# Kernel tuning notes

Measured on AMD Instinct MI355X. Metric: run time of the kernel, lower is better.

Reference implementation:

```python
import jax, jax.numpy as jnp
import numpy as np

N_STUDENT = 100000
N_COURSE = 20000
N_EDGES = 1000000
HIDDEN = 128


def setup_inputs() -> dict:
    key = jax.random.key(0)
    ks = jax.random.split(key, 8)
    scale = 1.0 / np.sqrt(2 * HIDDEN)
    return {
        "z_student": jax.random.normal(ks[0], (N_STUDENT, HIDDEN), dtype=jnp.float32),
        "z_course": jax.random.normal(ks[1], (N_COURSE, HIDDEN), dtype=jnp.float32),
        "row": jax.random.randint(ks[2], (N_EDGES,), 0, N_STUDENT, dtype=jnp.int64),
        "col": jax.random.randint(ks[3], (N_EDGES,), 0, N_COURSE, dtype=jnp.int64),
        "W1": jax.random.normal(ks[4], (2 * HIDDEN, HIDDEN), dtype=jnp.float32) * scale,
        "b1": jnp.zeros((HIDDEN,), dtype=jnp.float32),
        "W2": jax.random.normal(ks[5], (HIDDEN, 1), dtype=jnp.float32) * (1.0 / np.sqrt(HIDDEN)),
        "b2": jnp.zeros((1,), dtype=jnp.float32),
    }


def reference(z_student, z_course, row, col, W1, b1, W2, b2):
    # gather endpoint embeddings and concat along feature dim: [E, 2H]
    z = jnp.concatenate([z_student[row], z_course[col]], axis=-1)
    h = jax.nn.relu(z @ W1 + b1)   # [E, H]
    out = h @ W2 + b2              # [E, 1]
    return out.reshape(-1)
```

## Files before the change

kernel.cpp:

```cpp
#include <hip/hip_runtime.h>
#include <hip/hip_bf16.h>
#include <hip/hip_fp16.h>


typedef _Float16 half2v __attribute__((ext_vector_type(2)));
typedef _Float16 half8v __attribute__((ext_vector_type(8)));
typedef __fp16   fp16x2 __attribute__((ext_vector_type(2)));
typedef float    float4v __attribute__((ext_vector_type(4)));

#define NB   64
#define NR   16
#define CAPS 1152

__global__ __launch_bounds__(256) void conv_w(const float* __restrict__ W1,
                                              const float* __restrict__ W2,
                                              _Float16* __restrict__ Wt,
                                              _Float16* __restrict__ w2h,
                                              int* __restrict__ cnt) {
    int b = blockIdx.x, t = threadIdx.x;
    if (b == 8) {
        if (t < 128) w2h[t] = (_Float16)W2[t];
        for (int i = t; i < NB * NR; i += 256) cnt[i] = 0;
        return;
    }
    __shared__ _Float16 lds[32][136];
    int h = b >> 2, n0 = (b & 3) * 32;
    for (int i = 0; i < 16; ++i) {
        int idx = i * 256 + t;
        int k = idx >> 5, nn = idx & 31;
        lds[nn][k] = (_Float16)W1[(h * 128 + k) * 128 + n0 + nn];
    }
    __syncthreads();
    for (int j = 0; j < 2; ++j) {
        int idx = j * 256 + t;
        int nn = idx >> 4, kc = idx & 15;
        half8v v;
        #pragma unroll
        for (int q = 0; q < 8; ++q) v[q] = lds[nn][kc * 8 + q];
        *(half8v*)&Wt[((h * 128 + n0 + nn) * 128) + kc * 8] = v;
    }
}

__global__ __launch_bounds__(256) void gemm_scatter(
    const float* __restrict__ Zs, const float* __restrict__ Zc,
    const _Float16* __restrict__ Wt, const float* __restrict__ b1,
    _Float16* __restrict__ Us, _Float16* __restrict__ Uc,
    int Ms, int Mc, int nbs, int G,
    const int* __restrict__ row, const int* __restrict__ col,
    unsigned* __restrict__ rcB, int* __restrict__ pos,
    int* __restrict__ cnt, int E, float scale)
{
    __shared__ uint4 ldsW[2048];
    const int t = threadIdx.x;

    if ((int)blockIdx.x >= G) {
        const int sb = blockIdx.x - G;
        int* hist  = (int*)ldsW;
        int* base  = hist + NB;
        int* hist2 = hist + 2 * NB;
        const int rep = sb & (NR - 1);
        if (t < NB) { hist[t] = 0; hist2[t] = 0; }
        __syncthreads();
        const long e0 = (long)sb * 1024 + t;
        int r[4], c[4], bk[4];
        bool v[4];
        #pragma unroll
        for (int k = 0; k < 4; ++k) {
            long e = e0 + k * 256;
            v[k] = e < (long)E;
            long ee = v[k] ? e : 0;
            r[k] = __builtin_nontemporal_load(&row[ee]);
            c[k] = __builtin_nontemporal_load(&col[ee]);
            int b = (int)((float)r[k] * scale);
            bk[k] = b > NB - 1 ? NB - 1 : b;
            if (v[k]) atomicAdd(&hist[bk[k]], 1);
        }
        __syncthreads();
        if (t < NB) base[t] = atomicAdd(&cnt[t * NR + rep], hist[t]);
        __syncthreads();
        #pragma unroll
        for (int k = 0; k < 4; ++k) {
            if (!v[k]) continue;
            int o = atomicAdd(&hist2[bk[k]], 1);
            int slot = base[bk[k]] + o;
            long e = e0 + k * 256;
            int p = -1;
            if (slot < CAPS) {
                int g = (bk[k] * NR + rep) * CAPS + slot;
                unsigned packed = (unsigned)r[k] | ((unsigned)c[k] << 17);
                __builtin_nontemporal_store(packed, &rcB[g]);
                p = g;
            }
            __builtin_nontemporal_store(p, &pos[e]);
        }
        return;
    }

    const int bid = blockIdx.x;
    const float* Z; _Float16* U; const _Float16* W; int M, m0, addB;
    if (bid < nbs) { Z = Zs; U = Us; M = Ms; m0 = bid * 64;         W = Wt;         addB = 1; }
    else           { Z = Zc; U = Uc; M = Mc; m0 = (bid - nbs) * 64; W = Wt + 16384; addB = 0; }

    const uint4* Wv = (const uint4*)W;
    #pragma unroll
    for (int i = 0; i < 8; ++i) {
        int j = i * 256 + t;
        int n = j >> 4, ch = j & 15;
        ldsW[n * 16 + (ch ^ ((n >> 3) & 7))] = Wv[j];
    }
    __syncthreads();

    const int wave = t >> 6, lane = t & 63, quad = lane >> 4, l16 = lane & 15;
    int mrow = m0 + wave * 16 + l16;
    int mload = mrow < M ? mrow : M - 1;
    const float* zrow = Z + (long)mload * 128;

    float4v acc[8];
    #pragma unroll
    for (int nt = 0; nt < 8; ++nt) acc[nt] = (float4v)(0.0f);

    #pragma unroll
    for (int c = 0; c < 4; ++c) {
        const float4v* pa = (const float4v*)(zrow + c * 32 + quad * 8);
        float4v a0 = pa[0], a1 = pa[1];
        fp16x2 p[4];
        p[0] = __builtin_amdgcn_cvt_pkrtz(a0[0], a0[1]);
        p[1] = __builtin_amdgcn_cvt_pkrtz(a0[2], a0[3]);
        p[2] = __builtin_amdgcn_cvt_pkrtz(a1[0], a1[1]);
        p[3] = __builtin_amdgcn_cvt_pkrtz(a1[2], a1[3]);
        half8v af;
        __builtin_memcpy(&af, &p[0], 16);
        const int ch = c * 4 + quad;
        #pragma unroll
        for (int nt = 0; nt < 8; ++nt) {
            const int n = l16 * 8 + nt;
            const half8v* pb = (const half8v*)&ldsW[n * 16 + (ch ^ (l16 & 7))];
            acc[nt] = __builtin_amdgcn_mfma_f32_16x16x32_f16(af, *pb, acc[nt], 0, 0, 0);
        }
    }

    float bv[8];
    if (addB) {
        const float4v* pb1 = (const float4v*)(b1 + l16 * 8);
        float4v x0 = pb1[0], x1 = pb1[1];
        bv[0]=x0[0]; bv[1]=x0[1]; bv[2]=x0[2]; bv[3]=x0[3];
        bv[4]=x1[0]; bv[5]=x1[1]; bv[6]=x1[2]; bv[7]=x1[3];
    } else {
        #pragma unroll
        for (int i = 0; i < 8; ++i) bv[i] = 0.0f;
    }

    const int rbase = m0 + wave * 16 + quad * 4;
    #pragma unroll
    for (int r = 0; r < 4; ++r) {
        int rr = rbase + r;
        if (rr < M) {
            half8v o;
            #pragma unroll
            for (int nt = 0; nt < 8; ++nt) o[nt] = (_Float16)(acc[nt][r] + bv[nt]);
            *(half8v*)&U[(long)rr * 128 + l16 * 8] = o;
        }
    }
}

__global__ __launch_bounds__(256) void edge_bucket(
    const unsigned* __restrict__ rcB, const int* __restrict__ cnt,
    const _Float16* __restrict__ us, const _Float16* __restrict__ uc,
    const _Float16* __restrict__ w2h, const float* __restrict__ b2,
    float* __restrict__ outB)
{
    const int t = threadIdx.x, sub = t & 7, tg = t >> 3;
    const int x = blockIdx.x & 7;
    const int l = blockIdx.x >> 3;
    const int p = l & (NR - 1);
    const int w = l >> 4;

    const uint4* pw = (const uint4*)(w2h + sub * 16);
    uint4 w0 = pw[0], w1 = pw[1];
    half2v W[8];
    *(uint4*)&W[0] = w0; *(uint4*)&W[4] = w1;
    const float bb = b2[0];
    const half2v zero = {(_Float16)0, (_Float16)0};

    #pragma unroll 1
    for (int bl = 0; bl < NB / 8; ++bl) {
        const int b = x * (NB / 8) + bl;
        const int ss = b * NR + p;
        int n = cnt[ss]; n = n < CAPS ? n : CAPS;
        const int seg = ss * CAPS;
        #pragma unroll 1
        for (int i0 = w * 64; i0 < n; i0 += 16 * 64) {
            int i  = i0 + tg;
            int i2 = i + 32;
            bool a0v = i < n, a1v = i2 < n;
            int ii  = a0v ? i  : 0;
            int ii2 = a1v ? i2 : 0;
            unsigned p0 = __builtin_nontemporal_load(&rcB[seg + ii]);
            unsigned p1 = __builtin_nontemporal_load(&rcB[seg + ii2]);
            int r0 = p0 & 0x1FFFF, c0 = p0 >> 17;
            int r1 = p1 & 0x1FFFF, c1 = p1 >> 17;
            const uint4* pa0 = (const uint4*)(us + (long)r0 * 128 + sub * 16);
            const uint4* pb0 = (const uint4*)(uc + (long)c0 * 128 + sub * 16);
            const uint4* pa1 = (const uint4*)(us + (long)r1 * 128 + sub * 16);
            const uint4* pb1 = (const uint4*)(uc + (long)c1 * 128 + sub * 16);
            uint4 a00 = pa0[0], a01 = pa0[1];
            uint4 b00 = pb0[0], b01 = pb0[1];
            uint4 a10 = pa1[0], a11 = pa1[1];
            uint4 b10 = pb1[0], b11 = pb1[1];
            half2v A0[8], B0[8], A1[8], B1[8];
            *(uint4*)&A0[0] = a00; *(uint4*)&A0[4] = a01;
            *(uint4*)&B0[0] = b00; *(uint4*)&B0[4] = b01;
            *(uint4*)&A1[0] = a10; *(uint4*)&A1[4] = a11;
            *(uint4*)&B1[0] = b10; *(uint4*)&B1[4] = b11;
            float s0 = 0.0f, s1 = 0.0f;
            #pragma unroll
            for (int q = 0; q < 8; ++q) {
                half2v h0 = A0[q] + B0[q];
                half2v h1 = A1[q] + B1[q];
                h0 = __builtin_elementwise_max(h0, zero);
                h1 = __builtin_elementwise_max(h1, zero);
                s0 += (float)h0[0] * (float)W[q][0];
                s0 += (float)h0[1] * (float)W[q][1];
                s1 += (float)h1[0] * (float)W[q][0];
                s1 += (float)h1[1] * (float)W[q][1];
            }
            s0 += __shfl_xor(s0, 1);
            s1 += __shfl_xor(s1, 1);
            s0 += __shfl_xor(s0, 2);
            s1 += __shfl_xor(s1, 2);
            s0 += __shfl_xor(s0, 4);
            s1 += __shfl_xor(s1, 4);
            if (sub == 0) {
                if (a0v) outB[seg + i]  = s0 + bb;
                if (a1v) outB[seg + i2] = s1 + bb;
            }
        }
    }
}

__global__ __launch_bounds__(256) void unscatter(
    const int* __restrict__ pos, const float* __restrict__ outB,
    const int* __restrict__ row, const int* __restrict__ col,
    const _Float16* __restrict__ us, const _Float16* __restrict__ uc,
    const _Float16* __restrict__ w2h, const float* __restrict__ b2,
    float* __restrict__ out, int E)
{
    const int t = threadIdx.x;
    #pragma unroll
    for (int k = 0; k < 4; ++k) {
        long e = (long)blockIdx.x * 1024 + k * 256 + t;
        if (e >= (long)E) return;
        int p = __builtin_nontemporal_load(&pos[e]);
        float s;
        if (p >= 0) {
            s = outB[p];
        } else {
            int r = row[e], c = col[e];
            s = b2[0];
            for (int kk = 0; kk < 128; ++kk) {
                float h = (float)us[(long)r * 128 + kk] + (float)uc[(long)c * 128 + kk];
                s += fmaxf(h, 0.0f) * (float)w2h[kk];
            }
        }
        __builtin_nontemporal_store(s, &out[e]);
    }
}

__global__ __launch_bounds__(256) void edge_kernel(
    const int* __restrict__ row, const int* __restrict__ col,
    const _Float16* __restrict__ us, const _Float16* __restrict__ uc,
    const _Float16* __restrict__ w2h, const float* __restrict__ b2,
    float* __restrict__ out, int E)
{
    const int t = threadIdx.x;
    const int sub = t & 7;
    long e = (long)blockIdx.x * 32 + (t >> 3);
    if (e >= E) return;
    int r = row[e], c = col[e];

    const uint4* pa = (const uint4*)(us  + (long)r * 128 + sub * 16);
    const uint4* pb = (const uint4*)(uc  + (long)c * 128 + sub * 16);
    const uint4* pw = (const uint4*)(w2h + sub * 16);
    uint4 a0 = pa[0], a1 = pa[1];
    uint4 c0 = pb[0], c1 = pb[1];
    uint4 w0 = pw[0], w1 = pw[1];

    half2v A[8], B[8], W[8];
    *(uint4*)&A[0] = a0; *(uint4*)&A[4] = a1;
    *(uint4*)&B[0] = c0; *(uint4*)&B[4] = c1;
    *(uint4*)&W[0] = w0; *(uint4*)&W[4] = w1;

    const half2v zero = {(_Float16)0, (_Float16)0};
    float s = 0.0f;
    #pragma unroll
    for (int i = 0; i < 8; ++i) {
        half2v h = A[i] + B[i];
        h = __builtin_elementwise_max(h, zero);
        s += (float)h[0] * (float)W[i][0];
        s += (float)h[1] * (float)W[i][1];
    }
    s += __shfl_xor(s, 1);
    s += __shfl_xor(s, 2);
    s += __shfl_xor(s, 4);
    if (sub == 0) out[e] = s + b2[0];
}

extern "C" void kernel_launch(void* const* d_in, const int* in_sizes, int n_in,
                              void* d_out, int out_size, void* d_ws, size_t ws_size,
                              hipStream_t stream) {
    const float* zs  = (const float*)d_in[0];
    const float* zc  = (const float*)d_in[1];
    const int*   row = (const int*)d_in[2];
    const int*   col = (const int*)d_in[3];
    const float* W1  = (const float*)d_in[4];
    const float* b1  = (const float*)d_in[5];
    const float* W2  = (const float*)d_in[6];
    const float* b2  = (const float*)d_in[7];
    float* out = (float*)d_out;

    const int Ms = in_sizes[0] / 128;
    const int Mc = in_sizes[1] / 128;
    const int E  = in_sizes[2];

    char* wsb = (char*)d_ws;
    _Float16* Wt  = (_Float16*)wsb;
    _Float16* w2h = (_Float16*)(wsb + 65536);
    int*      cnt = (int*)(wsb + 65792);
    size_t off = 69888;
    _Float16* us = (_Float16*)(wsb + off);  off += (size_t)Ms * 256;
    _Float16* uc = (_Float16*)(wsb + off);  off += (size_t)Mc * 256;
    unsigned* rcB = (unsigned*)(wsb + off); off += (size_t)NB * NR * CAPS * 4;
    int*   pos  = (int*)(wsb + off);   off += (size_t)E * 4;
    float* outB = (float*)(wsb + off); off += (size_t)NB * NR * CAPS * 4;
    const bool bucketed = (off <= ws_size);

    const int nbs = (Ms + 63) / 64, nbc = (Mc + 63) / 64;
    const int G = nbs + nbc;
    const int SB = bucketed ? (E + 1023) / 1024 : 0;

    conv_w<<<9, 256, 0, stream>>>(W1, W2, Wt, w2h, cnt);
    gemm_scatter<<<G + SB, 256, 0, stream>>>(
        zs, zc, Wt, b1, us, uc, Ms, Mc, nbs, G,
        row, col, rcB, pos, cnt, E, (float)NB / (float)Ms);
    if (bucketed) {
        edge_bucket<<<2048, 256, 0, stream>>>(rcB, cnt, us, uc, w2h, b2, outB);
        unscatter<<<(E + 1023) / 1024, 256, 0, stream>>>(
            pos, outB, row, col, us, uc, w2h, b2, out, E);
    } else {
        edge_kernel<<<(E + 31) / 32, 256, 0, stream>>>(row, col, us, uc, w2h, b2, out, E);
    }
    (void)n_in; (void)out_size;
}
```

Measured before the change: 189.1 us.

## Split scatter from GEMM kernel and use more bucket replicas with smaller capacity

Moves the edge bucketing scatter out of the fused GEMM kernel into its own bucket_scatter launch, so it uses small static LDS instead of the GEMM's 32 KB weight tile. Bucket replicas go from 16 to 64 with per-segment capacity cut from 1152 to 384, spreading global counter atomics and shrinking the segments each edge_bucket block walks. The edge_bucket work split is adjusted to match. The rcB store becomes a normal store. The cost is losing the overlap between scatter and GEMM blocks, plus one extra launch.

```diff
diff --git a/kernel.cpp b/kernel.cpp
--- a/kernel.cpp
+++ b/kernel.cpp
@@ -9,8 +9,8 @@
 typedef float    float4v __attribute__((ext_vector_type(4)));
 
 #define NB   64
-#define NR   16
-#define CAPS 1152
+#define NR   64
+#define CAPS 384
 
 __global__ __launch_bounds__(256) void conv_w(const float* __restrict__ W1,
                                               const float* __restrict__ W2,
@@ -41,62 +41,15 @@
     }
 }
 
-__global__ __launch_bounds__(256) void gemm_scatter(
+__global__ __launch_bounds__(256) void gemm_u(
     const float* __restrict__ Zs, const float* __restrict__ Zc,
     const _Float16* __restrict__ Wt, const float* __restrict__ b1,
     _Float16* __restrict__ Us, _Float16* __restrict__ Uc,
-    int Ms, int Mc, int nbs, int G,
-    const int* __restrict__ row, const int* __restrict__ col,
-    unsigned* __restrict__ rcB, int* __restrict__ pos,
-    int* __restrict__ cnt, int E, float scale)
+    int Ms, int Mc, int nbs)
 {
     __shared__ uint4 ldsW[2048];
-    const int t = threadIdx.x;
-
-    if ((int)blockIdx.x >= G) {
-        const int sb = blockIdx.x - G;
-        int* hist  = (int*)ldsW;
-        int* base  = hist + NB;
-        int* hist2 = hist + 2 * NB;
-        const int rep = sb & (NR - 1);
-        if (t < NB) { hist[t] = 0; hist2[t] = 0; }
-        __syncthreads();
-        const long e0 = (long)sb * 1024 + t;
-        int r[4], c[4], bk[4];
-        bool v[4];
-        #pragma unroll
-        for (int k = 0; k < 4; ++k) {
-            long e = e0 + k * 256;
-            v[k] = e < (long)E;
-            long ee = v[k] ? e : 0;
-            r[k] = __builtin_nontemporal_load(&row[ee]);
-            c[k] = __builtin_nontemporal_load(&col[ee]);
-            int b = (int)((float)r[k] * scale);
-            bk[k] = b > NB - 1 ? NB - 1 : b;
-            if (v[k]) atomicAdd(&hist[bk[k]], 1);
-        }
-        __syncthreads();
-        if (t < NB) base[t] = atomicAdd(&cnt[t * NR + rep], hist[t]);
-        __syncthreads();
-        #pragma unroll
-        for (int k = 0; k < 4; ++k) {
-            if (!v[k]) continue;
-            int o = atomicAdd(&hist2[bk[k]], 1);
-            int slot = base[bk[k]] + o;
-            long e = e0 + k * 256;
-            int p = -1;
-            if (slot < CAPS) {
-                int g = (bk[k] * NR + rep) * CAPS + slot;
-                unsigned packed = (unsigned)r[k] | ((unsigned)c[k] << 17);
-                __builtin_nontemporal_store(packed, &rcB[g]);
-                p = g;
-            }
-            __builtin_nontemporal_store(p, &pos[e]);
-        }
-        return;
-    }
-
-    const int bid = blockIdx.x;
+    const int bid = blockIdx.x, t = threadIdx.x;
+
     const float* Z; _Float16* U; const _Float16* W; int M, m0, addB;
     if (bid < nbs) { Z = Zs; U = Us; M = Ms; m0 = bid * 64;         W = Wt;         addB = 1; }
     else           { Z = Zc; U = Uc; M = Mc; m0 = (bid - nbs) * 64; W = Wt + 16384; addB = 0; }
@@ -163,6 +116,49 @@
     }
 }
 
+__global__ __launch_bounds__(256) void bucket_scatter(
+    const int* __restrict__ row, const int* __restrict__ col,
+    unsigned* __restrict__ rcB, int* __restrict__ pos,
+    int* __restrict__ cnt, int E, float scale)
+{
+    __shared__ int hist[NB], base[NB], hist2[NB];
+    const int t = threadIdx.x;
+    const int rep = blockIdx.x & (NR - 1);
+    if (t < NB) { hist[t] = 0; hist2[t] = 0; }
+    __syncthreads();
+    const long e0 = (long)blockIdx.x * 1024 + t;
+    int r[4], c[4], bk[4];
+    bool v[4];
+    #pragma unroll
+    for (int k = 0; k < 4; ++k) {
+        long e = e0 + k * 256;
+        v[k] = e < (long)E;
+        long ee = v[k] ? e : 0;
+        r[k] = __builtin_nontemporal_load(&row[ee]);
+        c[k] = __builtin_nontemporal_load(&col[ee]);
+        int b = (int)((float)r[k] * scale);
+        bk[k] = b > NB - 1 ? NB - 1 : b;
+        if (v[k]) atomicAdd(&hist[bk[k]], 1);
+    }
+    __syncthreads();
+    if (t < NB) base[t] = atomicAdd(&cnt[t * NR + rep], hist[t]);
+    __syncthreads();
+    #pragma unroll
+    for (int k = 0; k < 4; ++k) {
+        if (!v[k]) continue;
+        int o = atomicAdd(&hist2[bk[k]], 1);
+        int slot = base[bk[k]] + o;
+        long e = e0 + k * 256;
+        int p = -1;
+        if (slot < CAPS) {
+            int g = (bk[k] * NR + rep) * CAPS + slot;
+            rcB[g] = (unsigned)r[k] | ((unsigned)c[k] << 17);
+            p = g;
+        }
+        __builtin_nontemporal_store(p, &pos[e]);
+    }
+}
+
 __global__ __launch_bounds__(256) void edge_bucket(
     const unsigned* __restrict__ rcB, const int* __restrict__ cnt,
     const _Float16* __restrict__ us, const _Float16* __restrict__ uc,
@@ -173,7 +169,7 @@
     const int x = blockIdx.x & 7;
     const int l = blockIdx.x >> 3;
     const int p = l & (NR - 1);
-    const int w = l >> 4;
+    const int w = l >> 6;
 
     const uint4* pw = (const uint4*)(w2h + sub * 16);
     uint4 w0 = pw[0], w1 = pw[1];
@@ -189,7 +185,7 @@
         int n = cnt[ss]; n = n < CAPS ? n : CAPS;
         const int seg = ss * CAPS;
         #pragma unroll 1
-        for (int i0 = w * 64; i0 < n; i0 += 16 * 64) {
+        for (int i0 = w * 64; i0 < n; i0 += 4 * 64) {
             int i  = i0 + tg;
             int i2 = i + 32;
             bool a0v = i < n, a1v = i2 < n;
@@ -326,7 +322,7 @@
     _Float16* Wt  = (_Float16*)wsb;
     _Float16* w2h = (_Float16*)(wsb + 65536);
     int*      cnt = (int*)(wsb + 65792);
-    size_t off = 69888;
+    size_t off = 65792 + 16384;
     _Float16* us = (_Float16*)(wsb + off);  off += (size_t)Ms * 256;
     _Float16* uc = (_Float16*)(wsb + off);  off += (size_t)Mc * 256;
     unsigned* rcB = (unsigned*)(wsb + off); off += (size_t)NB * NR * CAPS * 4;
@@ -335,14 +331,12 @@
     const bool bucketed = (off <= ws_size);
 
     const int nbs = (Ms + 63) / 64, nbc = (Mc + 63) / 64;
-    const int G = nbs + nbc;
-    const int SB = bucketed ? (E + 1023) / 1024 : 0;
 
     conv_w<<<9, 256, 0, stream>>>(W1, W2, Wt, w2h, cnt);
-    gemm_scatter<<<G + SB, 256, 0, stream>>>(
-        zs, zc, Wt, b1, us, uc, Ms, Mc, nbs, G,
-        row, col, rcB, pos, cnt, E, (float)NB / (float)Ms);
+    gemm_u<<<nbs + nbc, 256, 0, stream>>>(zs, zc, Wt, b1, us, uc, Ms, Mc, nbs);
     if (bucketed) {
+        bucket_scatter<<<(E + 1023) / 1024, 256, 0, stream>>>(
+            row, col, rcB, pos, cnt, E, (float)NB / (float)Ms);
         edge_bucket<<<2048, 256, 0, stream>>>(rcB, cnt, us, uc, w2h, b2, outB);
         unscatter<<<(E + 1023) / 1024, 256, 0, stream>>>(
             pos, outB, row, col, us, uc, w2h, b2, out, E);
```

Measured after the change: 176.1 us. -6.8%, faster.
